# Performance work log

Hardware: AMD Instinct MI355X
Metric: run time of the kernel (lower is better)

Reference implementation:

```python
import jax, jax.numpy as jnp
import numpy as np

B, N, D, H = 4, 2048, 1024, 16
HD = D // H
SCALE = HD ** -0.5

def neg_softmax(x):
    # sign(x) * softmax(|x|) along last axis
    return jnp.sign(x) * jax.nn.softmax(jnp.abs(x), axis=-1)

def setup_inputs() -> dict:
    key = jax.random.key(0)
    ks = jax.random.split(key, 9)
    s = 0.02
    return {
        "x": jax.random.normal(ks[0], (B, N, D), jnp.float32),
        "Wq": jax.random.normal(ks[1], (D, D), jnp.float32) * s,
        "bq": jax.random.normal(ks[2], (D,), jnp.float32) * s,
        "Wk": jax.random.normal(ks[3], (D, D), jnp.float32) * s,
        "bk": jax.random.normal(ks[4], (D,), jnp.float32) * s,
        "Wv": jax.random.normal(ks[5], (D, D), jnp.float32) * s,
        "bv": jax.random.normal(ks[6], (D,), jnp.float32) * s,
        "Wo": jax.random.normal(ks[7], (D, D), jnp.float32) * s,
        "bo": jax.random.normal(ks[8], (D,), jnp.float32) * s,
    }

def reference(x, Wq, bq, Wk, bk, Wv, bv, Wo, bo):
    def heads(t):  # [B,N,D] -> [B,H,N,hd]
        return t.reshape(B, N, H, HD).transpose(0, 2, 1, 3)
    Q = heads(x @ Wq.T + bq)
    K = heads(x @ Wk.T + bk)
    V = heads(x @ Wv.T + bv)
    logits = jnp.einsum('bhnd,bhmd->bhnm', Q, K) * SCALE
    attn = neg_softmax(logits)
    out = jnp.einsum('bhnm,bhmd->bhnd', attn, V)
    out = out.transpose(0, 2, 1, 3).reshape(B, N, D)
    return out @ Wo.T + bo
```

## Files before the change

kernel.cpp:

```cpp
#include <hip/hip_runtime.h>

typedef _Float16 f16x8 __attribute__((ext_vector_type(8)));
typedef __fp16 h16x2 __attribute__((ext_vector_type(2)));
typedef float f32x4 __attribute__((ext_vector_type(4)));
typedef unsigned short u16x4 __attribute__((ext_vector_type(4)));

#define NB 4
#define NSEQ 2048
#define NH 16
#define HDIM 64
#define DM 1024
#define MROWS (NB * NSEQ)

#define AS1 __attribute__((address_space(1)))
#define AS3 __attribute__((address_space(3)))

__device__ __forceinline__ float exp2_fast(float x) {
  float r; asm("v_exp_f32 %0, %1" : "=v"(r) : "v"(x)); return r;
}

__device__ __forceinline__ unsigned short f2h(float f) {
  _Float16 h = (_Float16)f;
  union { _Float16 h; unsigned short u; } v; v.h = h;
  return v.u;
}

__global__ void cvt_kernel(const float* __restrict__ in, unsigned short* __restrict__ out, int n4) {
  int i = blockIdx.x * blockDim.x + threadIdx.x;
  if (i < n4) {
    const float4 v = ((const float4*)in)[i];
    u16x4 o;
    o.x = f2h(v.x); o.y = f2h(v.y); o.z = f2h(v.z); o.w = f2h(v.w);
    ((u16x4*)out)[i] = o;
  }
}

__global__ void cvt4_kernel(const float* __restrict__ w0, const float* __restrict__ w1,
                            const float* __restrict__ w2, const float* __restrict__ w3,
                            unsigned short* __restrict__ o0, unsigned short* __restrict__ o1,
                            unsigned short* __restrict__ o2, unsigned short* __restrict__ o3) {
  const int i = blockIdx.x * blockDim.x + threadIdx.x;
  const float* src; unsigned short* dst;
  switch (blockIdx.y) {
    case 0: src = w0; dst = o0; break;
    case 1: src = w1; dst = o1; break;
    case 2: src = w2; dst = o2; break;
    default: src = w3; dst = o3; break;
  }
  const float4 v = ((const float4*)src)[i];
  u16x4 o;
  o.x = f2h(v.x); o.y = f2h(v.y); o.z = f2h(v.z); o.w = f2h(v.w);
  ((u16x4*)dst)[i] = o;
}

template<int OUT_F16>
__global__ __launch_bounds__(256)
void gemm_bt(const unsigned short* __restrict__ A, const unsigned short* __restrict__ Bw,
             const float* __restrict__ bias, void* __restrict__ Cv, float scale) {
  __shared__ unsigned short As[128 * 32];
  __shared__ unsigned short Bs[128 * 32];
  const int tid = threadIdx.x, lane = tid & 63, wave = tid >> 6;
  const int g = lane >> 4, c = lane & 15;
  const int orig = blockIdx.y * 8 + blockIdx.x;
  const int wg = (orig & 7) * 64 + (orig >> 3);
  const int m0 = (wg >> 3) * 128, n0 = (wg & 7) * 128;
  const int wm = (wave >> 1) * 64, wn = (wave & 1) * 64;
  f32x4 acc[4][4] = {};
  for (int kt = 0; kt < 1024; kt += 32) {
#pragma unroll
    for (int p = 0; p < 2; ++p) {
      const int idx = p * 256 + tid;
      const int row = idx >> 2, col = (idx & 3) * 8;
      __builtin_amdgcn_global_load_lds(
          (const AS1 void*)(A + (size_t)(m0 + row) * 1024 + kt + col),
          (AS3 void*)(As + idx * 8), 16, 0, 0);
      __builtin_amdgcn_global_load_lds(
          (const AS1 void*)(Bw + (size_t)(n0 + row) * 1024 + kt + col),
          (AS3 void*)(Bs + idx * 8), 16, 0, 0);
    }
    __syncthreads();
    f16x8 af[4], bfr[4];
#pragma unroll
    for (int i = 0; i < 4; ++i) af[i] = *(const f16x8*)(As + (wm + i * 16 + c) * 32 + g * 8);
#pragma unroll
    for (int i = 0; i < 4; ++i) bfr[i] = *(const f16x8*)(Bs + (wn + i * 16 + c) * 32 + g * 8);
#pragma unroll
    for (int i = 0; i < 4; ++i)
#pragma unroll
      for (int j = 0; j < 4; ++j)
        acc[i][j] = __builtin_amdgcn_mfma_f32_16x16x32_f16(af[i], bfr[j], acc[i][j], 0, 0, 0);
    __syncthreads();
  }
#pragma unroll
  for (int i = 0; i < 4; ++i)
#pragma unroll
    for (int j = 0; j < 4; ++j)
#pragma unroll
      for (int r = 0; r < 4; ++r) {
        const int row = m0 + wm + i * 16 + g * 4 + r;
        const int col = n0 + wn + j * 16 + c;
        const float v = (acc[i][j][r] + bias[col]) * scale;
        if (OUT_F16) ((unsigned short*)Cv)[(size_t)row * 1024 + col] = f2h(v);
        else         ((float*)Cv)[(size_t)row * 1024 + col] = v;
      }
}

__global__ __launch_bounds__(256, 3)
void attn_kernel(const unsigned short* __restrict__ Qg, const unsigned short* __restrict__ Kg,
                 const unsigned short* __restrict__ Vg, unsigned short* __restrict__ Og) {
  __shared__ __align__(16) unsigned short Kl[2][64 * 64];
  __shared__ __align__(16) unsigned short Vt[2][64 * 72];
  const int tid = threadIdx.x, lane = tid & 63, wave = tid >> 6;
  const int g = lane >> 4, c = lane & 15;
  const int orig = blockIdx.y * 16 + blockIdx.x;
  const int wg = (orig & 7) * 128 + (orig >> 3);
  const int qblk = wg & 15, bh = wg >> 4;
  const int b = bh >> 4, h = bh & 15;
  const int q0 = qblk * 128 + wave * 32;
  const size_t rb = (size_t)b * NSEQ;
  const int hc = h * HDIM;
  const int NT = NSEQ / 64;

  const int k_kvo = tid >> 3;
  const int k_d   = (((tid & 7) ^ ((tid >> 3) & 7)) * 8);
  const int v_kv = lane;
  const int pv = (v_kv & 32) | (((v_kv >> 2) & 3) << 3) | (((v_kv >> 4) & 1) << 2) | (v_kv & 3);

  f16x8 qf[2][2];
#pragma unroll
  for (int m = 0; m < 2; ++m)
#pragma unroll
    for (int kb2 = 0; kb2 < 2; ++kb2)
      qf[m][kb2] = *(const f16x8*)(Qg + (rb + q0 + m * 16 + c) * DM + hc + kb2 * 32 + g * 8);

  f32x4 oT[4][2] = {};
  float dpart[2] = {0.f, 0.f};
  f16x8 vreg[2];

  auto stageK = [&](int t, int buf) {
    const int kv0 = t * 64;
#pragma unroll
    for (int p = 0; p < 2; ++p) {
      const int kv = kv0 + 32 * p + k_kvo;
      __builtin_amdgcn_global_load_lds(
          (const AS1 void*)(Kg + (rb + kv) * DM + hc + k_d),
          (AS3 void*)(&Kl[buf][p * 2048 + tid * 8]), 16, 0, 0);
    }
  };
  auto loadV = [&](int t) {
    const int kv0 = t * 64;
#pragma unroll
    for (int p = 0; p < 2; ++p)
      vreg[p] = *(const f16x8*)(Vg + (rb + kv0 + v_kv) * DM + hc + p * 32 + wave * 8);
  };
  auto writeV = [&](int buf) {
#pragma unroll
    for (int p = 0; p < 2; ++p) {
      const int vd = p * 32 + wave * 8;
      union { f16x8 v; unsigned short u[8]; } vv; vv.v = vreg[p];
#pragma unroll
      for (int j = 0; j < 8; ++j) Vt[buf][(vd + j) * 72 + pv] = vv.u[j];
    }
  };

  stageK(0, 0);
  loadV(0);
  writeV(0);
  __syncthreads();

  for (int t = 0; t < NT; ++t) {
    const int cur = t & 1;
    if (t + 1 < NT) { stageK(t + 1, cur ^ 1); loadV(t + 1); }

    const unsigned short* KL = Kl[cur];
    const unsigned short* VT = Vt[cur];

    f16x8 kf[2][4];
#pragma unroll
    for (int kb2 = 0; kb2 < 2; ++kb2)
#pragma unroll
      for (int nb = 0; nb < 4; ++nb)
        kf[kb2][nb] = *(const f16x8*)(KL + (nb * 16 + c) * 64 + (((kb2 * 32 + g * 8) ^ ((c & 7) * 8))));
    f32x4 s[2][4] = {};
#pragma unroll
    for (int m = 0; m < 2; ++m)
#pragma unroll
      for (int nb = 0; nb < 4; ++nb)
#pragma unroll
        for (int kb2 = 0; kb2 < 2; ++kb2)
          s[m][nb] = __builtin_amdgcn_mfma_f32_16x16x32_f16(kf[kb2][nb], qf[m][kb2], s[m][nb], 0, 0, 0);

    f16x8 vtf[2][4];
#pragma unroll
    for (int kb2 = 0; kb2 < 2; ++kb2)
#pragma unroll
      for (int db = 0; db < 4; ++db)
        vtf[kb2][db] = *(const f16x8*)(VT + (db * 16 + c) * 72 + kb2 * 32 + g * 8);

#pragma unroll
    for (int m = 0; m < 2; ++m) {
      union PW { f16x8 v; h16x2 w[4]; } pf[2];
      float es = 0.f;
#pragma unroll
      for (int nb = 0; nb < 4; ++nb) {
        float p[4];
#pragma unroll
        for (int r = 0; r < 4; ++r) {
          const float sv = s[m][nb][r];
          const float e = exp2_fast(fabsf(sv) - 18.0f);
          es += e;
          p[r] = copysignf(e, sv);
        }
        pf[nb >> 1].w[(nb & 1) * 2]     = __builtin_amdgcn_cvt_pkrtz(p[0], p[1]);
        pf[nb >> 1].w[(nb & 1) * 2 + 1] = __builtin_amdgcn_cvt_pkrtz(p[2], p[3]);
      }
      dpart[m] += es;
#pragma unroll
      for (int db = 0; db < 4; ++db) {
        oT[db][m] = __builtin_amdgcn_mfma_f32_16x16x32_f16(vtf[0][db], pf[0].v, oT[db][m], 0, 0, 0);
        oT[db][m] = __builtin_amdgcn_mfma_f32_16x16x32_f16(vtf[1][db], pf[1].v, oT[db][m], 0, 0, 0);
      }
    }

    if (t + 1 < NT) writeV(cur ^ 1);
    __syncthreads();
  }

#pragma unroll
  for (int m = 0; m < 2; ++m) {
    float d = dpart[m];
    d += __shfl_xor(d, 16);
    d += __shfl_xor(d, 32);
    const float inv = 1.f / d;
#pragma unroll
    for (int db = 0; db < 4; ++db) {
      h16x2 h01 = __builtin_amdgcn_cvt_pkrtz(oT[db][m][0] * inv, oT[db][m][1] * inv);
      h16x2 h23 = __builtin_amdgcn_cvt_pkrtz(oT[db][m][2] * inv, oT[db][m][3] * inv);
      union { h16x2 h; unsigned u; } a, bb; a.h = h01; bb.h = h23;
      union { uint2 u2; unsigned u[2]; } st;
      st.u[0] = a.u; st.u[1] = bb.u;
      *(uint2*)(Og + (rb + q0 + m * 16 + c) * DM + hc + db * 16 + g * 4) = st.u2;
    }
  }
}

extern "C" void kernel_launch(void* const* d_in, const int* in_sizes, int n_in,
                              void* d_out, int out_size, void* d_ws, size_t ws_size,
                              hipStream_t stream) {
  const float* x  = (const float*)d_in[0];
  const float* Wq = (const float*)d_in[1];
  const float* bq = (const float*)d_in[2];
  const float* Wk = (const float*)d_in[3];
  const float* bk = (const float*)d_in[4];
  const float* Wv = (const float*)d_in[5];
  const float* bv = (const float*)d_in[6];
  const float* Wo = (const float*)d_in[7];
  const float* bo = (const float*)d_in[8];
  float* out = (float*)d_out;

  unsigned short* xb  = (unsigned short*)d_ws;
  unsigned short* wqb = xb  + (size_t)MROWS * DM;
  unsigned short* wkb = wqb + (size_t)DM * DM;
  unsigned short* wvb = wkb + (size_t)DM * DM;
  unsigned short* wob = wvb + (size_t)DM * DM;
  unsigned short* qb  = wob + (size_t)DM * DM;
  unsigned short* kb  = qb  + (size_t)MROWS * DM;
  unsigned short* vb  = kb  + (size_t)MROWS * DM;
  unsigned short* ab  = xb;

  cvt_kernel<<<(MROWS * DM) / 1024, 256, 0, stream>>>(x, xb, (MROWS * DM) / 4);
  cvt4_kernel<<<dim3((DM * DM) / 1024, 4), 256, 0, stream>>>(Wq, Wk, Wv, Wo, wqb, wkb, wvb, wob);

  const dim3 gg(DM / 128, MROWS / 128);
  const float SC = 0.125f * 1.4426950408889634f;
  gemm_bt<1><<<gg, 256, 0, stream>>>(xb, wqb, bq, qb, SC);
  gemm_bt<1><<<gg, 256, 0, stream>>>(xb, wkb, bk, kb, 1.f);
  gemm_bt<1><<<gg, 256, 0, stream>>>(xb, wvb, bv, vb, 1.f);

  attn_kernel<<<dim3(NSEQ / 128, NB * NH), 256, 0, stream>>>(qb, kb, vb, ab);

  gemm_bt<0><<<gg, 256, 0, stream>>>(ab, wob, bo, out, 1.f);
}
```

Before: 225.3 us.

## Split attention block into eight waves of sixteen query rows each

Result: no change. 226.5 us (+0.5%).

```diff
diff --git a/kernel.cpp b/kernel.cpp
--- a/kernel.cpp
+++ b/kernel.cpp
@@ -105,7 +105,7 @@
       }
 }
 
-__global__ __launch_bounds__(256, 3)
+__global__ __launch_bounds__(512, 4)
 void attn_kernel(const unsigned short* __restrict__ Qg, const unsigned short* __restrict__ Kg,
                  const unsigned short* __restrict__ Vg, unsigned short* __restrict__ Og) {
   __shared__ __align__(16) unsigned short Kl[2][64 * 64];
@@ -116,7 +116,7 @@
   const int wg = (orig & 7) * 128 + (orig >> 3);
   const int qblk = wg & 15, bh = wg >> 4;
   const int b = bh >> 4, h = bh & 15;
-  const int q0 = qblk * 128 + wave * 32;
+  const int q0 = qblk * 128 + wave * 16;
   const size_t rb = (size_t)b * NSEQ;
   const int hc = h * HDIM;
   const int NT = NSEQ / 64;
@@ -125,42 +125,30 @@
   const int k_d   = (((tid & 7) ^ ((tid >> 3) & 7)) * 8);
   const int v_kv = lane;
   const int pv = (v_kv & 32) | (((v_kv >> 2) & 3) << 3) | (((v_kv >> 4) & 1) << 2) | (v_kv & 3);
-
-  f16x8 qf[2][2];
-#pragma unroll
-  for (int m = 0; m < 2; ++m)
-#pragma unroll
-    for (int kb2 = 0; kb2 < 2; ++kb2)
-      qf[m][kb2] = *(const f16x8*)(Qg + (rb + q0 + m * 16 + c) * DM + hc + kb2 * 32 + g * 8);
-
-  f32x4 oT[4][2] = {};
-  float dpart[2] = {0.f, 0.f};
-  f16x8 vreg[2];
+  const int vd = wave * 8;
+
+  f16x8 qf[2];
+#pragma unroll
+  for (int kb2 = 0; kb2 < 2; ++kb2)
+    qf[kb2] = *(const f16x8*)(Qg + (rb + q0 + c) * DM + hc + kb2 * 32 + g * 8);
+
+  f32x4 oT[4] = {};
+  float dpart = 0.f;
+  f16x8 vreg;
 
   auto stageK = [&](int t, int buf) {
-    const int kv0 = t * 64;
-#pragma unroll
-    for (int p = 0; p < 2; ++p) {
-      const int kv = kv0 + 32 * p + k_kvo;
-      __builtin_amdgcn_global_load_lds(
-          (const AS1 void*)(Kg + (rb + kv) * DM + hc + k_d),
-          (AS3 void*)(&Kl[buf][p * 2048 + tid * 8]), 16, 0, 0);
-    }
+    const int kv = t * 64 + k_kvo;
+    __builtin_amdgcn_global_load_lds(
+        (const AS1 void*)(Kg + (rb + kv) * DM + hc + k_d),
+        (AS3 void*)(&Kl[buf][tid * 8]), 16, 0, 0);
   };
   auto loadV = [&](int t) {
-    const int kv0 = t * 64;
-#pragma unroll
-    for (int p = 0; p < 2; ++p)
-      vreg[p] = *(const f16x8*)(Vg + (rb + kv0 + v_kv) * DM + hc + p * 32 + wave * 8);
+    vreg = *(const f16x8*)(Vg + (rb + t * 64 + v_kv) * DM + hc + vd);
   };
   auto writeV = [&](int buf) {
-#pragma unroll
-    for (int p = 0; p < 2; ++p) {
-      const int vd = p * 32 + wave * 8;
-      union { f16x8 v; unsigned short u[8]; } vv; vv.v = vreg[p];
-#pragma unroll
-      for (int j = 0; j < 8; ++j) Vt[buf][(vd + j) * 72 + pv] = vv.u[j];
-    }
+    union { f16x8 v; unsigned short u[8]; } vv; vv.v = vreg;
+#pragma unroll
+    for (int j = 0; j < 8; ++j) Vt[buf][(vd + j) * 72 + pv] = vv.u[j];
   };
 
   stageK(0, 0);
@@ -181,14 +169,12 @@
 #pragma unroll
       for (int nb = 0; nb < 4; ++nb)
         kf[kb2][nb] = *(const f16x8*)(KL + (nb * 16 + c) * 64 + (((kb2 * 32 + g * 8) ^ ((c & 7) * 8))));
-    f32x4 s[2][4] = {};
-#pragma unroll
-    for (int m = 0; m < 2; ++m)
-#pragma unroll
-      for (int nb = 0; nb < 4; ++nb)
-#pragma unroll
-        for (int kb2 = 0; kb2 < 2; ++kb2)
-          s[m][nb] = __builtin_amdgcn_mfma_f32_16x16x32_f16(kf[kb2][nb], qf[m][kb2], s[m][nb], 0, 0, 0);
+    f32x4 s[4] = {};
+#pragma unroll
+    for (int nb = 0; nb < 4; ++nb)
+#pragma unroll
+      for (int kb2 = 0; kb2 < 2; ++kb2)
+        s[nb] = __builtin_amdgcn_mfma_f32_16x16x32_f16(kf[kb2][nb], qf[kb2], s[nb], 0, 0, 0);
 
     f16x8 vtf[2][4];
 #pragma unroll
@@ -197,50 +183,48 @@
       for (int db = 0; db < 4; ++db)
         vtf[kb2][db] = *(const f16x8*)(VT + (db * 16 + c) * 72 + kb2 * 32 + g * 8);
 
-#pragma unroll
-    for (int m = 0; m < 2; ++m) {
-      union PW { f16x8 v; h16x2 w[4]; } pf[2];
-      float es = 0.f;
-#pragma unroll
-      for (int nb = 0; nb < 4; ++nb) {
-        float p[4];
-#pragma unroll
-        for (int r = 0; r < 4; ++r) {
-          const float sv = s[m][nb][r];
-          const float e = exp2_fast(fabsf(sv) - 18.0f);
-          es += e;
-          p[r] = copysignf(e, sv);
-        }
-        pf[nb >> 1].w[(nb & 1) * 2]     = __builtin_amdgcn_cvt_pkrtz(p[0], p[1]);
-        pf[nb >> 1].w[(nb & 1) * 2 + 1] = __builtin_amdgcn_cvt_pkrtz(p[2], p[3]);
+    union PW { f16x8 v; h16x2 w[4]; } pf[2];
+    float es = 0.f;
+#pragma unroll
+    for (int nb = 0; nb < 4; ++nb) {
+      float p[4];
+#pragma unroll
+      for (int r = 0; r < 4; ++r) {
+        const float sv = s[nb][r];
+        const float e = exp2_fast(fabsf(sv) - 18.0f);
+        es += e;
+        p[r] = copysignf(e, sv);
       }
-      dpart[m] += es;
-#pragma unroll
-      for (int db = 0; db < 4; ++db) {
-        oT[db][m] = __builtin_amdgcn_mfma_f32_16x16x32_f16(vtf[0][db], pf[0].v, oT[db][m], 0, 0, 0);
-        oT[db][m] = __builtin_amdgcn_mfma_f32_16x16x32_f16(vtf[1][db], pf[1].v, oT[db][m], 0, 0, 0);
-      }
+      pf[nb >> 1].w[(nb & 1) * 2]     = __builtin_amdgcn_cvt_pkrtz(p[0], p[1]);
+      pf[nb >> 1].w[(nb & 1) * 2 + 1] = __builtin_amdgcn_cvt_pkrtz(p[2], p[3]);
+    }
+    dpart += es;
+
+    asm volatile("s_waitcnt lgkmcnt(0)" ::: "memory");
+    __builtin_amdgcn_sched_barrier(0);
+
+#pragma unroll
+    for (int db = 0; db < 4; ++db) {
+      oT[db] = __builtin_amdgcn_mfma_f32_16x16x32_f16(vtf[0][db], pf[0].v, oT[db], 0, 0, 0);
+      oT[db] = __builtin_amdgcn_mfma_f32_16x16x32_f16(vtf[1][db], pf[1].v, oT[db], 0, 0, 0);
     }
 
     if (t + 1 < NT) writeV(cur ^ 1);
     __syncthreads();
   }
 
-#pragma unroll
-  for (int m = 0; m < 2; ++m) {
-    float d = dpart[m];
-    d += __shfl_xor(d, 16);
-    d += __shfl_xor(d, 32);
-    const float inv = 1.f / d;
-#pragma unroll
-    for (int db = 0; db < 4; ++db) {
-      h16x2 h01 = __builtin_amdgcn_cvt_pkrtz(oT[db][m][0] * inv, oT[db][m][1] * inv);
-      h16x2 h23 = __builtin_amdgcn_cvt_pkrtz(oT[db][m][2] * inv, oT[db][m][3] * inv);
-      union { h16x2 h; unsigned u; } a, bb; a.h = h01; bb.h = h23;
-      union { uint2 u2; unsigned u[2]; } st;
-      st.u[0] = a.u; st.u[1] = bb.u;
-      *(uint2*)(Og + (rb + q0 + m * 16 + c) * DM + hc + db * 16 + g * 4) = st.u2;
-    }
+  float d = dpart;
+  d += __shfl_xor(d, 16);
+  d += __shfl_xor(d, 32);
+  const float inv = 1.f / d;
+#pragma unroll
+  for (int db = 0; db < 4; ++db) {
+    h16x2 h01 = __builtin_amdgcn_cvt_pkrtz(oT[db][0] * inv, oT[db][1] * inv);
+    h16x2 h23 = __builtin_amdgcn_cvt_pkrtz(oT[db][2] * inv, oT[db][3] * inv);
+    union { h16x2 h; unsigned u; } a, bb; a.h = h01; bb.h = h23;
+    union { uint2 u2; unsigned u[2]; } st;
+    st.u[0] = a.u; st.u[1] = bb.u;
+    *(uint2*)(Og + (rb + q0 + c) * DM + hc + db * 16 + g * 4) = st.u2;
   }
 }
 
@@ -277,7 +261,7 @@
   gemm_bt<1><<<gg, 256, 0, stream>>>(xb, wkb, bk, kb, 1.f);
   gemm_bt<1><<<gg, 256, 0, stream>>>(xb, wvb, bv, vb, 1.f);
 
-  attn_kernel<<<dim3(NSEQ / 128, NB * NH), 256, 0, stream>>>(qb, kb, vb, ab);
+  attn_kernel<<<dim3(NSEQ / 128, NB * NH), 512, 0, stream>>>(qb, kb, vb, ab);
 
   gemm_bt<0><<<gg, 256, 0, stream>>>(ab, wob, bo, out, 1.f);
 }
```
